# Kernel optimization log

Measured on AMD Instinct MI355X. Metric: run time of the kernel, lower is better.

## Reference

```python
import jax, jax.numpy as jnp
import numpy as np

N = 50000       # nodes
E_RAND = 800000 # random edges (avg degree ~16)
K = 64          # edges touching `node`; setup_inputs guarantees exactly K
F = 64          # num_node_features
C = 64          # conv_channels


def setup_inputs() -> dict:
    key = jax.random.key(0)
    ks = jax.random.split(key, 6)
    x = jax.random.normal(ks[0], (N, F), dtype=jnp.float32)
    # random edges avoiding node 0 so exactly the K prepended edges touch node 0
    src = jax.random.randint(ks[1], (E_RAND,), 1, N, dtype=jnp.int64)
    dst = jax.random.randint(ks[2], (E_RAND,), 1, N, dtype=jnp.int64)
    ksrc = jnp.zeros((K,), dtype=jnp.int64)
    kdst = jnp.arange(1, K + 1, dtype=jnp.int64)
    edge_index = jnp.stack([jnp.concatenate([ksrc, src]),
                            jnp.concatenate([kdst, dst])])  # [2, K+E_RAND]
    W1 = jax.random.normal(ks[3], (F, C), jnp.float32) / np.float32(np.sqrt(F))
    b1 = jnp.zeros((C,), jnp.float32)
    W2 = jax.random.normal(ks[4], (C, C), jnp.float32) / np.float32(np.sqrt(C))
    b2 = jnp.zeros((C,), jnp.float32)
    Wr = jax.random.normal(ks[5], (C, 1), jnp.float32) / np.float32(np.sqrt(C))
    br = jnp.zeros((1,), jnp.float32)
    return {"x": x, "edge_index": edge_index, "node": 0,
            "W1": W1, "b1": b1, "W2": W2, "b2": b2, "Wr": Wr, "br": br}


def gcn_conv(x, src, dst, W, b):
    """PyG GCNConv with self-loops already appended to (src, dst).
    out[v] = sum_{(u,v)} deg(u)^-1/2 * deg(v)^-1/2 * (x @ W)[u] + b
    """
    n = x.shape[0]
    xw = x @ W                                              # [N, C]
    deg = jnp.zeros((n,), xw.dtype).at[dst].add(1.0)        # in-degree incl. self-loop
    dinv = jnp.where(deg > 0, jax.lax.rsqrt(deg), 0.0)
    norm = dinv[src] * dinv[dst]                            # [E]
    out = jax.ops.segment_sum(xw[src] * norm[:, None], dst, num_segments=n)
    return out + b


def reference(x, edge_index, node, W1, b1, W2, b2, Wr, br):
    n = x.shape[0]
    loop = jnp.arange(n, dtype=edge_index.dtype)
    src = jnp.concatenate([edge_index[0], loop])  # add self loops (GCNConv default)
    dst = jnp.concatenate([edge_index[1], loop])
    h = jax.nn.relu(gcn_conv(x, src, dst, W1, b1))
    h = jax.nn.relu(gcn_conv(h, src, dst, W2, b2))
    # edges incident to `node` (setup guarantees exactly K such edges)
    s0, d0 = edge_index[0], edge_index[1]
    mask = (s0 == node) | (d0 == node)
    idx = jnp.nonzero(mask, size=K)[0]
    s, d = s0[idx], d0[idx]
    targets = jnp.where(s == node, d, s)  # self-loop (s==d==node) -> node
    score = h[targets] @ Wr + br          # [K, 1]
    score = jax.nn.softmax(score, axis=0)
    return score[:, 0], targets
```

## Files before the change

### kernel.cpp

```cpp
#include <hip/hip_runtime.h>
#include <math.h>

#define KK 64
#define CAP 64
#define NF 4160
#define HSZ 8192

__global__ __launch_bounds__(256) void k_find(const int* __restrict__ ei, int E,
                                              const int* __restrict__ nodep,
                                              int* __restrict__ cnt,
                                              int* __restrict__ tcount,
                                              int* __restrict__ tpairs,
                                              float* __restrict__ h1s) {
    int idx = blockIdx.x * 256 + threadIdx.x;
    if (idx < 64) h1s[(size_t)NF * 64 + idx] = 0.f;
    int node = nodep[0];
    int n4 = E >> 2;
    if (idx < n4) {
        int4 ss = ((const int4*)ei)[idx];
        int4 dd = ((const int4*)(ei + E))[idx];
        int s[4] = {ss.x, ss.y, ss.z, ss.w};
        int d[4] = {dd.x, dd.y, dd.z, dd.w};
#pragma unroll
        for (int k = 0; k < 4; k++) {
            atomicAdd(&cnt[d[k]], 1);
            if (s[k] == node || d[k] == node) {
                int q = atomicAdd(tcount, 1);
                if (q < KK) { int e = idx * 4 + k; tpairs[2 * q] = e; tpairs[2 * q + 1] = (s[k] == node) ? d[k] : s[k]; }
            }
        }
    }
    if (idx == 0) {
        for (int e = n4 * 4; e < E; e++) {
            int s = ei[e], d = ei[E + e];
            atomicAdd(&cnt[d], 1);
            if (s == node || d == node) {
                int q = atomicAdd(tcount, 1);
                if (q < KK) { tpairs[2 * q] = e; tpairs[2 * q + 1] = (s == node) ? d : s; }
            }
        }
    }
}

__global__ __launch_bounds__(256) void k_collect_t(const int* __restrict__ ei, int E,
                                                   const int* __restrict__ tpairs,
                                                   int* __restrict__ tcnt2,
                                                   int* __restrict__ tslots,
                                                   int* __restrict__ tsorted_g,
                                                   int* __restrict__ towner_g) {
    __shared__ unsigned char tflag[50048];
    __shared__ int eidx[KK], tgt[KK], srt[KK];
    int tid = threadIdx.x;
    for (int i = tid; i < 50048 / 16; i += 256) ((int4*)tflag)[i] = make_int4(0, 0, 0, 0);
    if (tid < KK) { eidx[tid] = tpairs[2 * tid]; tgt[tid] = tpairs[2 * tid + 1]; }
    __syncthreads();
    if (tid < KK) {
        int rank = 0;
        for (int j = 0; j < KK; j++) rank += (eidx[j] < eidx[tid]) ? 1 : 0;
        srt[rank] = tgt[tid];
    }
    __syncthreads();
    if (tid < KK) {
        int mynode = srt[tid];
        int owner = tid;
        for (int j = 0; j < tid; j++) if (srt[j] == mynode) { owner = j; break; }
        if (owner == tid) tflag[mynode] = (unsigned char)(tid + 1);
        if (blockIdx.x == 0) { tsorted_g[tid] = mynode; towner_g[tid] = owner; }
    }
    __syncthreads();
    int n4 = E >> 2;
    for (int idx = blockIdx.x * 256 + tid; idx < n4; idx += gridDim.x * 256) {
        int4 ss = ((const int4*)ei)[idx];
        int4 dd = ((const int4*)(ei + E))[idx];
        int s[4] = {ss.x, ss.y, ss.z, ss.w};
        int d[4] = {dd.x, dd.y, dd.z, dd.w};
#pragma unroll
        for (int k = 0; k < 4; k++) {
            int f = tflag[d[k]];
            if (f) { int p = atomicAdd(&tcnt2[f - 1], 1); if (p < CAP) tslots[(f - 1) * CAP + p] = s[k]; }
        }
    }
    if (blockIdx.x == 0 && tid == 0) {
        for (int e = n4 * 4; e < E; e++) {
            int f = tflag[ei[E + e]];
            if (f) { int p = atomicAdd(&tcnt2[f - 1], 1); if (p < CAP) tslots[(f - 1) * CAP + p] = ei[e]; }
        }
    }
}

__device__ __forceinline__ int fnode_of(int i, const int* tsorted, const int* towner,
                                        const int* tcnt2, const int* tslots) {
    int tp = i / 65, j = i % 65;
    if (j == 0) return tsorted[tp];
    int own = towner[tp];
    int c = tcnt2[own]; if (c > CAP) c = CAP;
    return (j - 1 < c) ? tslots[own * CAP + (j - 1)] : -1;
}

__global__ __launch_bounds__(256) void k_collect_f(const int* __restrict__ ei, int E,
                                                   const int* __restrict__ tsorted,
                                                   const int* __restrict__ towner,
                                                   const int* __restrict__ tcnt2,
                                                   const int* __restrict__ tslots,
                                                   int* __restrict__ fcnt,
                                                   int* __restrict__ fslots,
                                                   int* __restrict__ fnode_g,
                                                   int* __restrict__ fidx_g,
                                                   unsigned char* __restrict__ fown_g) {
    __shared__ unsigned int hmap[HSZ];
    int tid = threadIdx.x;
    for (int i = tid; i < HSZ; i += 256) hmap[i] = 0xFFFFFFFFu;
    __syncthreads();
    for (int i = tid; i < NF; i += 256) {
        int u = fnode_of(i, tsorted, towner, tcnt2, tslots);
        if (u >= 0) {
            unsigned int packed = ((unsigned)u << 16) | (unsigned)i;
            unsigned int slot = (((unsigned)u * 2654435761u) >> 13) & (HSZ - 1);
            while (true) {
                unsigned int cur = hmap[slot];
                if (cur == 0xFFFFFFFFu) {
                    unsigned int old = atomicCAS(&hmap[slot], 0xFFFFFFFFu, packed);
                    if (old == 0xFFFFFFFFu) break;
                    cur = old;
                }
                if ((cur >> 16) == (unsigned)u) {
                    if ((cur & 0xFFFFu) <= (unsigned)i) break;
                    if (atomicCAS(&hmap[slot], cur, packed) == cur) break;
                } else {
                    slot = (slot + 1) & (HSZ - 1);
                }
            }
        }
    }
    __syncthreads();
    if (blockIdx.x == 0) {
        for (int i = tid; i < NF; i += 256) {
            int u = fnode_of(i, tsorted, towner, tcnt2, tslots);
            int row = NF, isown = 0;
            if (u >= 0) {
                unsigned int slot = (((unsigned)u * 2654435761u) >> 13) & (HSZ - 1);
                while (true) {
                    unsigned int cur = hmap[slot];
                    if ((cur >> 16) == (unsigned)u) { row = (int)(cur & 0xFFFFu); break; }
                    slot = (slot + 1) & (HSZ - 1);
                }
                isown = (row == i);
            }
            fnode_g[i] = u; fidx_g[i] = row; fown_g[i] = (unsigned char)isown;
        }
    }
    int n4 = E >> 2;
    for (int idx = blockIdx.x * 256 + tid; idx < n4; idx += gridDim.x * 256) {
        int4 ss = ((const int4*)ei)[idx];
        int4 dd = ((const int4*)(ei + E))[idx];
        int s[4] = {ss.x, ss.y, ss.z, ss.w};
        int d[4] = {dd.x, dd.y, dd.z, dd.w};
#pragma unroll
        for (int k = 0; k < 4; k++) {
            unsigned int key = (unsigned)d[k];
            unsigned int slot = ((key * 2654435761u) >> 13) & (HSZ - 1);
            int row = -1;
            while (true) {
                unsigned int cur = hmap[slot];
                if (cur == 0xFFFFFFFFu) break;
                if ((cur >> 16) == key) { row = (int)(cur & 0xFFFFu); break; }
                slot = (slot + 1) & (HSZ - 1);
            }
            if (row >= 0) { int p = atomicAdd(&fcnt[row], 1); if (p < CAP) fslots[(size_t)row * CAP + p] = s[k]; }
        }
    }
    if (blockIdx.x == 0 && tid == 0) {
        for (int e = n4 * 4; e < E; e++) {
            unsigned int key = (unsigned)ei[E + e];
            unsigned int slot = ((key * 2654435761u) >> 13) & (HSZ - 1);
            int row = -1;
            while (true) {
                unsigned int cur = hmap[slot];
                if (cur == 0xFFFFFFFFu) break;
                if ((cur >> 16) == key) { row = (int)(cur & 0xFFFFu); break; }
                slot = (slot + 1) & (HSZ - 1);
            }
            if (row >= 0) { int p = atomicAdd(&fcnt[row], 1); if (p < CAP) fslots[(size_t)row * CAP + p] = ei[e]; }
        }
    }
}

__global__ __launch_bounds__(256) void k_layer1(const float* __restrict__ x,
                                                const int* __restrict__ fnode,
                                                const unsigned char* __restrict__ fown,
                                                const int* __restrict__ cnt,
                                                const int* __restrict__ fcnt,
                                                const int* __restrict__ fslots,
                                                const float* __restrict__ W1,
                                                const float* __restrict__ b1,
                                                float* __restrict__ h1s) {
    __shared__ __align__(16) float W1s[64 * 64];
    int tid = threadIdx.x;
    for (int i = tid; i < 1024; i += 256) ((float4*)W1s)[i] = ((const float4*)W1)[i];
    __syncthreads();
    int i = blockIdx.x * 4 + (tid >> 6);
    int lane = tid & 63;
    if (i >= NF) return;
    if (!fown[i]) return;
    int u = fnode[i];
    float du = rsqrtf((float)(cnt[u] + 1));
    float acc = du * x[(size_t)u * 64 + lane];
    int c = fcnt[i]; if (c > CAP) c = CAP;
    const int* sl = fslots + (size_t)i * CAP;
    int k = 0;
    for (; k + 4 <= c; k += 4) {
        int u0 = sl[k], u1 = sl[k + 1], u2 = sl[k + 2], u3 = sl[k + 3];
        float f0 = rsqrtf((float)(cnt[u0] + 1));
        float f1 = rsqrtf((float)(cnt[u1] + 1));
        float f2 = rsqrtf((float)(cnt[u2] + 1));
        float f3 = rsqrtf((float)(cnt[u3] + 1));
        acc += f0 * x[(size_t)u0 * 64 + lane] + f1 * x[(size_t)u1 * 64 + lane]
             + f2 * x[(size_t)u2 * 64 + lane] + f3 * x[(size_t)u3 * 64 + lane];
    }
    for (; k < c; k++) {
        int uu = sl[k];
        acc += rsqrtf((float)(cnt[uu] + 1)) * x[(size_t)uu * 64 + lane];
    }
    float z = du * acc;
    float h = 0.f;
#pragma unroll
    for (int f = 0; f < 64; f++) h += __shfl(z, f) * W1s[f * 64 + lane];
    h = fmaxf(h + b1[lane], 0.f);
    h1s[(size_t)i * 64 + lane] = du * h;
}

__global__ __launch_bounds__(64) void k_score2(const float* __restrict__ h1s,
                                               const int* __restrict__ fidx,
                                               const int* __restrict__ tsorted,
                                               const int* __restrict__ cnt,
                                               const float* __restrict__ W2,
                                               const float* __restrict__ b2,
                                               const float* __restrict__ Wr,
                                               float* __restrict__ sc) {
    int tp = blockIdx.x;
    int lane = threadIdx.x;
    int t = tsorted[tp];
    float dt = rsqrtf((float)(cnt[t] + 1));
    const int* fx = fidx + tp * 65;
    float z = 0.f;
#pragma unroll
    for (int j = 0; j < 65; j++) {
        int idx = fx[j];
        z += h1s[(size_t)idx * 64 + lane];
    }
    z *= dt;
    float acc = 0.f;
#pragma unroll
    for (int f = 0; f < 64; f++) acc += __shfl(z, f) * W2[f * 64 + lane];
    float h2 = fmaxf(acc + b2[lane], 0.f);
    float p = h2 * Wr[lane];
#pragma unroll
    for (int off = 32; off >= 1; off >>= 1) p += __shfl_xor(p, off);
    if (lane == 0) sc[tp] = p;
}

__global__ void k_softmax(const float* __restrict__ sc, const int* __restrict__ tsorted,
                          float* __restrict__ out) {
    int t = threadIdx.x;
    float s = sc[t];
    float m = s;
#pragma unroll
    for (int off = 32; off >= 1; off >>= 1) m = fmaxf(m, __shfl_xor(m, off));
    float e = __expf(s - m);
    float ss = e;
#pragma unroll
    for (int off = 32; off >= 1; off >>= 1) ss += __shfl_xor(ss, off);
    out[t] = e / ss;
    out[KK + t] = (float)tsorted[t];
}

extern "C" void kernel_launch(void* const* d_in, const int* in_sizes, int n_in,
                              void* d_out, int out_size, void* d_ws, size_t ws_size,
                              hipStream_t stream) {
    const float* x  = (const float*)d_in[0];
    const int*   ei = (const int*)d_in[1];
    const int*   nodep = (const int*)d_in[2];
    const float* W1 = (const float*)d_in[3];
    const float* b1 = (const float*)d_in[4];
    const float* W2 = (const float*)d_in[5];
    const float* b2 = (const float*)d_in[6];
    const float* Wr = (const float*)d_in[7];
    const float* br = (const float*)d_in[8];
    float* out = (float*)d_out;
    (void)br;

    int N = in_sizes[0] / 64;
    int E = in_sizes[1] / 2;

    char* w = (char*)d_ws;
    char* zstart = w;
    int* cnt    = (int*)w; w += (size_t)N * 4;
    int* tcnt2  = (int*)w; w += KK * 4;
    int* fcnt   = (int*)w; w += (size_t)NF * 4;
    int* tcount = (int*)w; w += 16;
    size_t zbytes = (size_t)(w - zstart);
    int* tpairs  = (int*)w; w += 2 * KK * 4;
    int* tsorted = (int*)w; w += KK * 4;
    int* towner  = (int*)w; w += KK * 4;
    int* tslots  = (int*)w; w += (size_t)KK * CAP * 4;
    int* fnode   = (int*)w; w += (size_t)NF * 4;
    int* fidx    = (int*)w; w += (size_t)NF * 4;
    unsigned char* fown = (unsigned char*)w; w += (size_t)NF;
    w = (char*)(((size_t)w + 15) & ~(size_t)15);
    int* fslots  = (int*)w; w += (size_t)NF * CAP * 4;
    float* h1s   = (float*)w; w += (size_t)(NF + 1) * 64 * 4;
    float* sc    = (float*)w; w += KK * 4;

    hipMemsetAsync(zstart, 0, zbytes, stream);

    int n4 = E >> 2;
    int ebl = (n4 + 255) / 256;
    k_find<<<ebl, 256, 0, stream>>>(ei, E, nodep, cnt, tcount, tpairs, h1s);
    k_collect_t<<<512, 256, 0, stream>>>(ei, E, tpairs, tcnt2, tslots, tsorted, towner);
    k_collect_f<<<512, 256, 0, stream>>>(ei, E, tsorted, towner, tcnt2, tslots,
                                         fcnt, fslots, fnode, fidx, fown);
    k_layer1<<<(NF + 3) / 4, 256, 0, stream>>>(x, fnode, fown, cnt, fcnt, fslots, W1, b1, h1s);
    k_score2<<<KK, 64, 0, stream>>>(h1s, fidx, tsorted, cnt, W2, b2, Wr, sc);
    k_softmax<<<1, 64, 0, stream>>>(sc, tsorted, out);
}
```

Before: 170.8 us.

## Fuse all stages into one cooperative persistent kernel with grid syncs

Replaces the memset plus six separate kernel launches with a single cooperative kernel of 256 blocks that runs every stage and separates them with grid.sync(). Workspace zeroing now happens inside the kernel. The goal is to remove launch gaps and the memset. In exchange, the edge-scan phases run on fewer blocks than before (256 instead of up to 512 or ~800), the large shared buffer limits occupancy, and the grid-wide barriers have their own cost.

```diff
diff --git a/kernel.cpp b/kernel.cpp
--- a/kernel.cpp
+++ b/kernel.cpp
@@ -1,92 +1,15 @@
 #include <hip/hip_runtime.h>
+#include <hip/hip_cooperative_groups.h>
 #include <math.h>
+
+namespace cg = cooperative_groups;
 
 #define KK 64
 #define CAP 64
 #define NF 4160
 #define HSZ 8192
-
-__global__ __launch_bounds__(256) void k_find(const int* __restrict__ ei, int E,
-                                              const int* __restrict__ nodep,
-                                              int* __restrict__ cnt,
-                                              int* __restrict__ tcount,
-                                              int* __restrict__ tpairs,
-                                              float* __restrict__ h1s) {
-    int idx = blockIdx.x * 256 + threadIdx.x;
-    if (idx < 64) h1s[(size_t)NF * 64 + idx] = 0.f;
-    int node = nodep[0];
-    int n4 = E >> 2;
-    if (idx < n4) {
-        int4 ss = ((const int4*)ei)[idx];
-        int4 dd = ((const int4*)(ei + E))[idx];
-        int s[4] = {ss.x, ss.y, ss.z, ss.w};
-        int d[4] = {dd.x, dd.y, dd.z, dd.w};
-#pragma unroll
-        for (int k = 0; k < 4; k++) {
-            atomicAdd(&cnt[d[k]], 1);
-            if (s[k] == node || d[k] == node) {
-                int q = atomicAdd(tcount, 1);
-                if (q < KK) { int e = idx * 4 + k; tpairs[2 * q] = e; tpairs[2 * q + 1] = (s[k] == node) ? d[k] : s[k]; }
-            }
-        }
-    }
-    if (idx == 0) {
-        for (int e = n4 * 4; e < E; e++) {
-            int s = ei[e], d = ei[E + e];
-            atomicAdd(&cnt[d], 1);
-            if (s == node || d == node) {
-                int q = atomicAdd(tcount, 1);
-                if (q < KK) { tpairs[2 * q] = e; tpairs[2 * q + 1] = (s == node) ? d : s; }
-            }
-        }
-    }
-}
-
-__global__ __launch_bounds__(256) void k_collect_t(const int* __restrict__ ei, int E,
-                                                   const int* __restrict__ tpairs,
-                                                   int* __restrict__ tcnt2,
-                                                   int* __restrict__ tslots,
-                                                   int* __restrict__ tsorted_g,
-                                                   int* __restrict__ towner_g) {
-    __shared__ unsigned char tflag[50048];
-    __shared__ int eidx[KK], tgt[KK], srt[KK];
-    int tid = threadIdx.x;
-    for (int i = tid; i < 50048 / 16; i += 256) ((int4*)tflag)[i] = make_int4(0, 0, 0, 0);
-    if (tid < KK) { eidx[tid] = tpairs[2 * tid]; tgt[tid] = tpairs[2 * tid + 1]; }
-    __syncthreads();
-    if (tid < KK) {
-        int rank = 0;
-        for (int j = 0; j < KK; j++) rank += (eidx[j] < eidx[tid]) ? 1 : 0;
-        srt[rank] = tgt[tid];
-    }
-    __syncthreads();
-    if (tid < KK) {
-        int mynode = srt[tid];
-        int owner = tid;
-        for (int j = 0; j < tid; j++) if (srt[j] == mynode) { owner = j; break; }
-        if (owner == tid) tflag[mynode] = (unsigned char)(tid + 1);
-        if (blockIdx.x == 0) { tsorted_g[tid] = mynode; towner_g[tid] = owner; }
-    }
-    __syncthreads();
-    int n4 = E >> 2;
-    for (int idx = blockIdx.x * 256 + tid; idx < n4; idx += gridDim.x * 256) {
-        int4 ss = ((const int4*)ei)[idx];
-        int4 dd = ((const int4*)(ei + E))[idx];
-        int s[4] = {ss.x, ss.y, ss.z, ss.w};
-        int d[4] = {dd.x, dd.y, dd.z, dd.w};
-#pragma unroll
-        for (int k = 0; k < 4; k++) {
-            int f = tflag[d[k]];
-            if (f) { int p = atomicAdd(&tcnt2[f - 1], 1); if (p < CAP) tslots[(f - 1) * CAP + p] = s[k]; }
-        }
-    }
-    if (blockIdx.x == 0 && tid == 0) {
-        for (int e = n4 * 4; e < E; e++) {
-            int f = tflag[ei[E + e]];
-            if (f) { int p = atomicAdd(&tcnt2[f - 1], 1); if (p < CAP) tslots[(f - 1) * CAP + p] = ei[e]; }
-        }
-    }
-}
+#define NB 256
+#define NT 256
 
 __device__ __forceinline__ int fnode_of(int i, const int* tsorted, const int* towner,
                                         const int* tcnt2, const int* tslots) {
@@ -97,181 +20,249 @@
     return (j - 1 < c) ? tslots[own * CAP + (j - 1)] : -1;
 }
 
-__global__ __launch_bounds__(256) void k_collect_f(const int* __restrict__ ei, int E,
-                                                   const int* __restrict__ tsorted,
-                                                   const int* __restrict__ towner,
-                                                   const int* __restrict__ tcnt2,
-                                                   const int* __restrict__ tslots,
-                                                   int* __restrict__ fcnt,
-                                                   int* __restrict__ fslots,
-                                                   int* __restrict__ fnode_g,
-                                                   int* __restrict__ fidx_g,
-                                                   unsigned char* __restrict__ fown_g) {
-    __shared__ unsigned int hmap[HSZ];
-    int tid = threadIdx.x;
-    for (int i = tid; i < HSZ; i += 256) hmap[i] = 0xFFFFFFFFu;
-    __syncthreads();
-    for (int i = tid; i < NF; i += 256) {
-        int u = fnode_of(i, tsorted, towner, tcnt2, tslots);
-        if (u >= 0) {
-            unsigned int packed = ((unsigned)u << 16) | (unsigned)i;
-            unsigned int slot = (((unsigned)u * 2654435761u) >> 13) & (HSZ - 1);
-            while (true) {
-                unsigned int cur = hmap[slot];
-                if (cur == 0xFFFFFFFFu) {
-                    unsigned int old = atomicCAS(&hmap[slot], 0xFFFFFFFFu, packed);
-                    if (old == 0xFFFFFFFFu) break;
-                    cur = old;
-                }
-                if ((cur >> 16) == (unsigned)u) {
-                    if ((cur & 0xFFFFu) <= (unsigned)i) break;
-                    if (atomicCAS(&hmap[slot], cur, packed) == cur) break;
-                } else {
-                    slot = (slot + 1) & (HSZ - 1);
-                }
-            }
-        }
-    }
-    __syncthreads();
-    if (blockIdx.x == 0) {
-        for (int i = tid; i < NF; i += 256) {
-            int u = fnode_of(i, tsorted, towner, tcnt2, tslots);
-            int row = NF, isown = 0;
-            if (u >= 0) {
-                unsigned int slot = (((unsigned)u * 2654435761u) >> 13) & (HSZ - 1);
-                while (true) {
-                    unsigned int cur = hmap[slot];
-                    if ((cur >> 16) == (unsigned)u) { row = (int)(cur & 0xFFFFu); break; }
-                    slot = (slot + 1) & (HSZ - 1);
-                }
-                isown = (row == i);
-            }
-            fnode_g[i] = u; fidx_g[i] = row; fown_g[i] = (unsigned char)isown;
-        }
-    }
+__global__ __launch_bounds__(NT) void k_mega(
+    const float* __restrict__ x, const int* __restrict__ ei, int E, int N,
+    const int* __restrict__ nodep,
+    const float* __restrict__ W1, const float* __restrict__ b1,
+    const float* __restrict__ W2, const float* __restrict__ b2,
+    const float* __restrict__ Wr,
+    int* cnt, int* tcount, int* tpairs,
+    int* tsorted_g, int* towner_g, int* tcnt2, int* tslots,
+    int* fnode_g, int* fidx_g, unsigned char* fown_g,
+    int* fcnt, int* fslots, float* h1s, float* sc, float* out)
+{
+    cg::grid_group grid = cg::this_grid();
+    __shared__ __align__(16) unsigned char smem[50048 + 1024];
+    int tid = threadIdx.x, bid = blockIdx.x;
+    int gidx = bid * NT + tid;
+    const int gstride = NB * NT;
     int n4 = E >> 2;
-    for (int idx = blockIdx.x * 256 + tid; idx < n4; idx += gridDim.x * 256) {
+
+    for (int i = gidx; i < N; i += gstride) cnt[i] = 0;
+    for (int i = gidx; i < NF; i += gstride) fcnt[i] = 0;
+    if (gidx < KK) tcnt2[gidx] = 0;
+    if (gidx == 0) *tcount = 0;
+    if (gidx < 64) h1s[(size_t)NF * 64 + gidx] = 0.f;
+    grid.sync();
+
+    int node = nodep[0];
+    for (int idx = gidx; idx < n4; idx += gstride) {
         int4 ss = ((const int4*)ei)[idx];
         int4 dd = ((const int4*)(ei + E))[idx];
         int s[4] = {ss.x, ss.y, ss.z, ss.w};
         int d[4] = {dd.x, dd.y, dd.z, dd.w};
 #pragma unroll
         for (int k = 0; k < 4; k++) {
-            unsigned int key = (unsigned)d[k];
-            unsigned int slot = ((key * 2654435761u) >> 13) & (HSZ - 1);
-            int row = -1;
-            while (true) {
-                unsigned int cur = hmap[slot];
-                if (cur == 0xFFFFFFFFu) break;
-                if ((cur >> 16) == key) { row = (int)(cur & 0xFFFFu); break; }
-                slot = (slot + 1) & (HSZ - 1);
-            }
-            if (row >= 0) { int p = atomicAdd(&fcnt[row], 1); if (p < CAP) fslots[(size_t)row * CAP + p] = s[k]; }
-        }
-    }
-    if (blockIdx.x == 0 && tid == 0) {
+            atomicAdd(&cnt[d[k]], 1);
+            if (s[k] == node || d[k] == node) {
+                int q = atomicAdd(tcount, 1);
+                if (q < KK) { int e = idx * 4 + k; tpairs[2 * q] = e; tpairs[2 * q + 1] = (s[k] == node) ? d[k] : s[k]; }
+            }
+        }
+    }
+    if (gidx == 0) {
         for (int e = n4 * 4; e < E; e++) {
-            unsigned int key = (unsigned)ei[E + e];
-            unsigned int slot = ((key * 2654435761u) >> 13) & (HSZ - 1);
-            int row = -1;
-            while (true) {
-                unsigned int cur = hmap[slot];
-                if (cur == 0xFFFFFFFFu) break;
-                if ((cur >> 16) == key) { row = (int)(cur & 0xFFFFu); break; }
-                slot = (slot + 1) & (HSZ - 1);
-            }
-            if (row >= 0) { int p = atomicAdd(&fcnt[row], 1); if (p < CAP) fslots[(size_t)row * CAP + p] = ei[e]; }
-        }
-    }
-}
-
-__global__ __launch_bounds__(256) void k_layer1(const float* __restrict__ x,
-                                                const int* __restrict__ fnode,
-                                                const unsigned char* __restrict__ fown,
-                                                const int* __restrict__ cnt,
-                                                const int* __restrict__ fcnt,
-                                                const int* __restrict__ fslots,
-                                                const float* __restrict__ W1,
-                                                const float* __restrict__ b1,
-                                                float* __restrict__ h1s) {
-    __shared__ __align__(16) float W1s[64 * 64];
-    int tid = threadIdx.x;
-    for (int i = tid; i < 1024; i += 256) ((float4*)W1s)[i] = ((const float4*)W1)[i];
-    __syncthreads();
-    int i = blockIdx.x * 4 + (tid >> 6);
-    int lane = tid & 63;
-    if (i >= NF) return;
-    if (!fown[i]) return;
-    int u = fnode[i];
-    float du = rsqrtf((float)(cnt[u] + 1));
-    float acc = du * x[(size_t)u * 64 + lane];
-    int c = fcnt[i]; if (c > CAP) c = CAP;
-    const int* sl = fslots + (size_t)i * CAP;
-    int k = 0;
-    for (; k + 4 <= c; k += 4) {
-        int u0 = sl[k], u1 = sl[k + 1], u2 = sl[k + 2], u3 = sl[k + 3];
-        float f0 = rsqrtf((float)(cnt[u0] + 1));
-        float f1 = rsqrtf((float)(cnt[u1] + 1));
-        float f2 = rsqrtf((float)(cnt[u2] + 1));
-        float f3 = rsqrtf((float)(cnt[u3] + 1));
-        acc += f0 * x[(size_t)u0 * 64 + lane] + f1 * x[(size_t)u1 * 64 + lane]
-             + f2 * x[(size_t)u2 * 64 + lane] + f3 * x[(size_t)u3 * 64 + lane];
-    }
-    for (; k < c; k++) {
-        int uu = sl[k];
-        acc += rsqrtf((float)(cnt[uu] + 1)) * x[(size_t)uu * 64 + lane];
-    }
-    float z = du * acc;
-    float h = 0.f;
-#pragma unroll
-    for (int f = 0; f < 64; f++) h += __shfl(z, f) * W1s[f * 64 + lane];
-    h = fmaxf(h + b1[lane], 0.f);
-    h1s[(size_t)i * 64 + lane] = du * h;
-}
-
-__global__ __launch_bounds__(64) void k_score2(const float* __restrict__ h1s,
-                                               const int* __restrict__ fidx,
-                                               const int* __restrict__ tsorted,
-                                               const int* __restrict__ cnt,
-                                               const float* __restrict__ W2,
-                                               const float* __restrict__ b2,
-                                               const float* __restrict__ Wr,
-                                               float* __restrict__ sc) {
-    int tp = blockIdx.x;
-    int lane = threadIdx.x;
-    int t = tsorted[tp];
-    float dt = rsqrtf((float)(cnt[t] + 1));
-    const int* fx = fidx + tp * 65;
-    float z = 0.f;
-#pragma unroll
-    for (int j = 0; j < 65; j++) {
-        int idx = fx[j];
-        z += h1s[(size_t)idx * 64 + lane];
-    }
-    z *= dt;
-    float acc = 0.f;
-#pragma unroll
-    for (int f = 0; f < 64; f++) acc += __shfl(z, f) * W2[f * 64 + lane];
-    float h2 = fmaxf(acc + b2[lane], 0.f);
-    float p = h2 * Wr[lane];
-#pragma unroll
-    for (int off = 32; off >= 1; off >>= 1) p += __shfl_xor(p, off);
-    if (lane == 0) sc[tp] = p;
-}
-
-__global__ void k_softmax(const float* __restrict__ sc, const int* __restrict__ tsorted,
-                          float* __restrict__ out) {
-    int t = threadIdx.x;
-    float s = sc[t];
-    float m = s;
-#pragma unroll
-    for (int off = 32; off >= 1; off >>= 1) m = fmaxf(m, __shfl_xor(m, off));
-    float e = __expf(s - m);
-    float ss = e;
-#pragma unroll
-    for (int off = 32; off >= 1; off >>= 1) ss += __shfl_xor(ss, off);
-    out[t] = e / ss;
-    out[KK + t] = (float)tsorted[t];
+            int s = ei[e], d = ei[E + e];
+            atomicAdd(&cnt[d], 1);
+            if (s == node || d == node) {
+                int q = atomicAdd(tcount, 1);
+                if (q < KK) { tpairs[2 * q] = e; tpairs[2 * q + 1] = (s == node) ? d : s; }
+            }
+        }
+    }
+    grid.sync();
+
+    {
+        unsigned char* tflag = smem;
+        int* eidx = (int*)(smem + 50048);
+        int* tgt = eidx + KK;
+        int* srt = tgt + KK;
+        for (int i = tid; i < 50048 / 16; i += NT) ((int4*)tflag)[i] = make_int4(0, 0, 0, 0);
+        if (tid < KK) { eidx[tid] = tpairs[2 * tid]; tgt[tid] = tpairs[2 * tid + 1]; }
+        __syncthreads();
+        if (tid < KK) {
+            int rank = 0;
+            for (int j = 0; j < KK; j++) rank += (eidx[j] < eidx[tid]) ? 1 : 0;
+            srt[rank] = tgt[tid];
+        }
+        __syncthreads();
+        if (tid < KK) {
+            int mynode = srt[tid];
+            int owner = tid;
+            for (int j = 0; j < tid; j++) if (srt[j] == mynode) { owner = j; break; }
+            if (owner == tid) tflag[mynode] = (unsigned char)(tid + 1);
+            if (bid == 0) { tsorted_g[tid] = mynode; towner_g[tid] = owner; }
+        }
+        __syncthreads();
+        for (int idx = gidx; idx < n4; idx += gstride) {
+            int4 ss = ((const int4*)ei)[idx];
+            int4 dd = ((const int4*)(ei + E))[idx];
+            int s[4] = {ss.x, ss.y, ss.z, ss.w};
+            int d[4] = {dd.x, dd.y, dd.z, dd.w};
+#pragma unroll
+            for (int k = 0; k < 4; k++) {
+                int f = tflag[d[k]];
+                if (f) { int p = atomicAdd(&tcnt2[f - 1], 1); if (p < CAP) tslots[(f - 1) * CAP + p] = s[k]; }
+            }
+        }
+        if (gidx == 0) {
+            for (int e = n4 * 4; e < E; e++) {
+                int f = tflag[ei[E + e]];
+                if (f) { int p = atomicAdd(&tcnt2[f - 1], 1); if (p < CAP) tslots[(f - 1) * CAP + p] = ei[e]; }
+            }
+        }
+    }
+    grid.sync();
+
+    {
+        unsigned int* hmap = (unsigned int*)smem;
+        for (int i = tid; i < HSZ; i += NT) hmap[i] = 0xFFFFFFFFu;
+        __syncthreads();
+        for (int i = tid; i < NF; i += NT) {
+            int u = fnode_of(i, tsorted_g, towner_g, tcnt2, tslots);
+            if (u >= 0) {
+                unsigned int packed = ((unsigned)u << 16) | (unsigned)i;
+                unsigned int slot = (((unsigned)u * 2654435761u) >> 13) & (HSZ - 1);
+                while (true) {
+                    unsigned int cur = hmap[slot];
+                    if (cur == 0xFFFFFFFFu) {
+                        unsigned int old = atomicCAS(&hmap[slot], 0xFFFFFFFFu, packed);
+                        if (old == 0xFFFFFFFFu) break;
+                        cur = old;
+                    }
+                    if ((cur >> 16) == (unsigned)u) {
+                        if ((cur & 0xFFFFu) <= (unsigned)i) break;
+                        if (atomicCAS(&hmap[slot], cur, packed) == cur) break;
+                    } else {
+                        slot = (slot + 1) & (HSZ - 1);
+                    }
+                }
+            }
+        }
+        __syncthreads();
+        if (bid == 0) {
+            for (int i = tid; i < NF; i += NT) {
+                int u = fnode_of(i, tsorted_g, towner_g, tcnt2, tslots);
+                int row = NF, isown = 0;
+                if (u >= 0) {
+                    unsigned int slot = (((unsigned)u * 2654435761u) >> 13) & (HSZ - 1);
+                    while (true) {
+                        unsigned int cur = hmap[slot];
+                        if ((cur >> 16) == (unsigned)u) { row = (int)(cur & 0xFFFFu); break; }
+                        slot = (slot + 1) & (HSZ - 1);
+                    }
+                    isown = (row == i);
+                }
+                fnode_g[i] = u; fidx_g[i] = row; fown_g[i] = (unsigned char)isown;
+            }
+        }
+        for (int idx = gidx; idx < n4; idx += gstride) {
+            int4 ss = ((const int4*)ei)[idx];
+            int4 dd = ((const int4*)(ei + E))[idx];
+            int s[4] = {ss.x, ss.y, ss.z, ss.w};
+            int d[4] = {dd.x, dd.y, dd.z, dd.w};
+#pragma unroll
+            for (int k = 0; k < 4; k++) {
+                unsigned int key = (unsigned)d[k];
+                unsigned int slot = ((key * 2654435761u) >> 13) & (HSZ - 1);
+                int row = -1;
+                while (true) {
+                    unsigned int cur = hmap[slot];
+                    if (cur == 0xFFFFFFFFu) break;
+                    if ((cur >> 16) == key) { row = (int)(cur & 0xFFFFu); break; }
+                    slot = (slot + 1) & (HSZ - 1);
+                }
+                if (row >= 0) { int p = atomicAdd(&fcnt[row], 1); if (p < CAP) fslots[(size_t)row * CAP + p] = s[k]; }
+            }
+        }
+        if (gidx == 0) {
+            for (int e = n4 * 4; e < E; e++) {
+                unsigned int key = (unsigned)ei[E + e];
+                unsigned int slot = ((key * 2654435761u) >> 13) & (HSZ - 1);
+                int row = -1;
+                while (true) {
+                    unsigned int cur = hmap[slot];
+                    if (cur == 0xFFFFFFFFu) break;
+                    if ((cur >> 16) == key) { row = (int)(cur & 0xFFFFu); break; }
+                    slot = (slot + 1) & (HSZ - 1);
+                }
+                if (row >= 0) { int p = atomicAdd(&fcnt[row], 1); if (p < CAP) fslots[(size_t)row * CAP + p] = ei[e]; }
+            }
+        }
+    }
+    grid.sync();
+
+    {
+        float* W1s = (float*)smem;
+        for (int i = tid; i < 1024; i += NT) ((float4*)W1s)[i] = ((const float4*)W1)[i];
+        __syncthreads();
+        int wv = tid >> 6, lane = tid & 63;
+        for (int i = bid * 4 + wv; i < NF; i += NB * 4) {
+            if (!fown_g[i]) continue;
+            int u = fnode_g[i];
+            float du = rsqrtf((float)(cnt[u] + 1));
+            float acc = du * x[(size_t)u * 64 + lane];
+            int c = fcnt[i]; if (c > CAP) c = CAP;
+            const int* sl = fslots + (size_t)i * CAP;
+            int k = 0;
+            for (; k + 4 <= c; k += 4) {
+                int u0 = sl[k], u1 = sl[k + 1], u2 = sl[k + 2], u3 = sl[k + 3];
+                float f0 = rsqrtf((float)(cnt[u0] + 1));
+                float f1 = rsqrtf((float)(cnt[u1] + 1));
+                float f2 = rsqrtf((float)(cnt[u2] + 1));
+                float f3 = rsqrtf((float)(cnt[u3] + 1));
+                acc += f0 * x[(size_t)u0 * 64 + lane] + f1 * x[(size_t)u1 * 64 + lane]
+                     + f2 * x[(size_t)u2 * 64 + lane] + f3 * x[(size_t)u3 * 64 + lane];
+            }
+            for (; k < c; k++) {
+                int uu = sl[k];
+                acc += rsqrtf((float)(cnt[uu] + 1)) * x[(size_t)uu * 64 + lane];
+            }
+            float z = du * acc;
+            float h = 0.f;
+#pragma unroll
+            for (int f = 0; f < 64; f++) h += __shfl(z, f) * W1s[f * 64 + lane];
+            h = fmaxf(h + b1[lane], 0.f);
+            h1s[(size_t)i * 64 + lane] = du * h;
+        }
+    }
+    grid.sync();
+
+    if (bid < KK && tid < 64) {
+        int tp = bid, lane = tid;
+        int t = tsorted_g[tp];
+        float dt = rsqrtf((float)(cnt[t] + 1));
+        const int* fx = fidx_g + tp * 65;
+        float z = 0.f;
+#pragma unroll
+        for (int j = 0; j < 65; j++) {
+            int idx = fx[j];
+            z += h1s[(size_t)idx * 64 + lane];
+        }
+        z *= dt;
+        float acc = 0.f;
+#pragma unroll
+        for (int f = 0; f < 64; f++) acc += __shfl(z, f) * W2[f * 64 + lane];
+        float h2 = fmaxf(acc + b2[lane], 0.f);
+        float p = h2 * Wr[lane];
+#pragma unroll
+        for (int off = 32; off >= 1; off >>= 1) p += __shfl_xor(p, off);
+        if (lane == 0) sc[tp] = p;
+    }
+    grid.sync();
+
+    if (bid == 0 && tid < KK) {
+        float s = sc[tid];
+        float m = s;
+#pragma unroll
+        for (int off = 32; off >= 1; off >>= 1) m = fmaxf(m, __shfl_xor(m, off));
+        float e = __expf(s - m);
+        float ss = e;
+#pragma unroll
+        for (int off = 32; off >= 1; off >>= 1) ss += __shfl_xor(ss, off);
+        out[tid] = e / ss;
+        out[KK + tid] = (float)tsorted_g[tid];
+    }
 }
 
 extern "C" void kernel_launch(void* const* d_in, const int* in_sizes, int n_in,
@@ -293,33 +284,27 @@
     int E = in_sizes[1] / 2;
 
     char* w = (char*)d_ws;
-    char* zstart = w;
-    int* cnt    = (int*)w; w += (size_t)N * 4;
-    int* tcnt2  = (int*)w; w += KK * 4;
-    int* fcnt   = (int*)w; w += (size_t)NF * 4;
-    int* tcount = (int*)w; w += 16;
-    size_t zbytes = (size_t)(w - zstart);
+    int* cnt     = (int*)w; w += (size_t)N * 4;
+    int* tcount  = (int*)w; w += 16;
     int* tpairs  = (int*)w; w += 2 * KK * 4;
     int* tsorted = (int*)w; w += KK * 4;
     int* towner  = (int*)w; w += KK * 4;
+    int* tcnt2   = (int*)w; w += KK * 4;
     int* tslots  = (int*)w; w += (size_t)KK * CAP * 4;
     int* fnode   = (int*)w; w += (size_t)NF * 4;
     int* fidx    = (int*)w; w += (size_t)NF * 4;
+    int* fcnt    = (int*)w; w += (size_t)NF * 4;
     unsigned char* fown = (unsigned char*)w; w += (size_t)NF;
     w = (char*)(((size_t)w + 15) & ~(size_t)15);
     int* fslots  = (int*)w; w += (size_t)NF * CAP * 4;
     float* h1s   = (float*)w; w += (size_t)(NF + 1) * 64 * 4;
     float* sc    = (float*)w; w += KK * 4;
 
-    hipMemsetAsync(zstart, 0, zbytes, stream);
-
-    int n4 = E >> 2;
-    int ebl = (n4 + 255) / 256;
-    k_find<<<ebl, 256, 0, stream>>>(ei, E, nodep, cnt, tcount, tpairs, h1s);
-    k_collect_t<<<512, 256, 0, stream>>>(ei, E, tpairs, tcnt2, tslots, tsorted, towner);
-    k_collect_f<<<512, 256, 0, stream>>>(ei, E, tsorted, towner, tcnt2, tslots,
-                                         fcnt, fslots, fnode, fidx, fown);
-    k_layer1<<<(NF + 3) / 4, 256, 0, stream>>>(x, fnode, fown, cnt, fcnt, fslots, W1, b1, h1s);
-    k_score2<<<KK, 64, 0, stream>>>(h1s, fidx, tsorted, cnt, W2, b2, Wr, sc);
-    k_softmax<<<1, 64, 0, stream>>>(sc, tsorted, out);
+    void* args[] = { (void*)&x, (void*)&ei, (void*)&E, (void*)&N, (void*)&nodep,
+                     (void*)&W1, (void*)&b1, (void*)&W2, (void*)&b2, (void*)&Wr,
+                     (void*)&cnt, (void*)&tcount, (void*)&tpairs,
+                     (void*)&tsorted, (void*)&towner, (void*)&tcnt2, (void*)&tslots,
+                     (void*)&fnode, (void*)&fidx, (void*)&fown,
+                     (void*)&fcnt, (void*)&fslots, (void*)&h1s, (void*)&sc, (void*)&out };
+    hipLaunchCooperativeKernel((const void*)k_mega, dim3(NB), dim3(NT), args, 0, stream);
 }
```

After: 332.8 us. +94.9%, slower.

## Split degree counting across collect kernels and shrink shared target flag to bitmask

Applied to the files above, without the earlier changes.

Moves the in-degree atomic counting out of the find kernel and splits it between the two collect kernels, each handling half of every int4 group, so the atomics overlap with edge scans that already happen. It replaces the 50KB byte flag array in shared memory with a 6KB bitmask plus a linear search over 64 target nodes, which should raise occupancy of the collect kernel. Zeroing of the count buffers is folded into the find kernel instead of a large memset. The risk is that the degree array is now read only after both collect kernels finish, and the bitmask hit path adds a 64-entry scan per hit.

```diff
diff --git a/kernel.cpp b/kernel.cpp
--- a/kernel.cpp
+++ b/kernel.cpp
@@ -5,14 +5,16 @@
 #define CAP 64
 #define NF 4160
 #define HSZ 8192
+#define BMW 1568
 
 __global__ __launch_bounds__(256) void k_find(const int* __restrict__ ei, int E,
                                               const int* __restrict__ nodep,
-                                              int* __restrict__ cnt,
+                                              int4* __restrict__ zbase, int zcount4,
                                               int* __restrict__ tcount,
                                               int* __restrict__ tpairs,
                                               float* __restrict__ h1s) {
     int idx = blockIdx.x * 256 + threadIdx.x;
+    if (idx < zcount4) zbase[idx] = make_int4(0, 0, 0, 0);
     if (idx < 64) h1s[(size_t)NF * 64 + idx] = 0.f;
     int node = nodep[0];
     int n4 = E >> 2;
@@ -23,7 +25,6 @@
         int d[4] = {dd.x, dd.y, dd.z, dd.w};
 #pragma unroll
         for (int k = 0; k < 4; k++) {
-            atomicAdd(&cnt[d[k]], 1);
             if (s[k] == node || d[k] == node) {
                 int q = atomicAdd(tcount, 1);
                 if (q < KK) { int e = idx * 4 + k; tpairs[2 * q] = e; tpairs[2 * q + 1] = (s[k] == node) ? d[k] : s[k]; }
@@ -33,7 +34,6 @@
     if (idx == 0) {
         for (int e = n4 * 4; e < E; e++) {
             int s = ei[e], d = ei[E + e];
-            atomicAdd(&cnt[d], 1);
             if (s == node || d == node) {
                 int q = atomicAdd(tcount, 1);
                 if (q < KK) { tpairs[2 * q] = e; tpairs[2 * q + 1] = (s == node) ? d : s; }
@@ -44,14 +44,16 @@
 
 __global__ __launch_bounds__(256) void k_collect_t(const int* __restrict__ ei, int E,
                                                    const int* __restrict__ tpairs,
+                                                   int* __restrict__ cnt,
                                                    int* __restrict__ tcnt2,
                                                    int* __restrict__ tslots,
                                                    int* __restrict__ tsorted_g,
                                                    int* __restrict__ towner_g) {
-    __shared__ unsigned char tflag[50048];
+    __shared__ unsigned int bmask[BMW];
+    __shared__ int tnode[KK];
     __shared__ int eidx[KK], tgt[KK], srt[KK];
     int tid = threadIdx.x;
-    for (int i = tid; i < 50048 / 16; i += 256) ((int4*)tflag)[i] = make_int4(0, 0, 0, 0);
+    for (int i = tid; i < BMW; i += 256) bmask[i] = 0u;
     if (tid < KK) { eidx[tid] = tpairs[2 * tid]; tgt[tid] = tpairs[2 * tid + 1]; }
     __syncthreads();
     if (tid < KK) {
@@ -64,7 +66,8 @@
         int mynode = srt[tid];
         int owner = tid;
         for (int j = 0; j < tid; j++) if (srt[j] == mynode) { owner = j; break; }
-        if (owner == tid) tflag[mynode] = (unsigned char)(tid + 1);
+        tnode[tid] = (owner == tid) ? mynode : -1;
+        if (owner == tid) atomicOr(&bmask[mynode >> 5], 1u << (mynode & 31));
         if (blockIdx.x == 0) { tsorted_g[tid] = mynode; towner_g[tid] = owner; }
     }
     __syncthreads();
@@ -74,16 +77,26 @@
         int4 dd = ((const int4*)(ei + E))[idx];
         int s[4] = {ss.x, ss.y, ss.z, ss.w};
         int d[4] = {dd.x, dd.y, dd.z, dd.w};
+        atomicAdd(&cnt[d[0]], 1);
+        atomicAdd(&cnt[d[1]], 1);
 #pragma unroll
         for (int k = 0; k < 4; k++) {
-            int f = tflag[d[k]];
-            if (f) { int p = atomicAdd(&tcnt2[f - 1], 1); if (p < CAP) tslots[(f - 1) * CAP + p] = s[k]; }
+            if ((bmask[d[k] >> 5] >> (d[k] & 31)) & 1u) {
+                int f = 0;
+                for (int j = 0; j < KK; j++) if (tnode[j] == d[k]) { f = j + 1; break; }
+                if (f) { int p = atomicAdd(&tcnt2[f - 1], 1); if (p < CAP) tslots[(f - 1) * CAP + p] = s[k]; }
+            }
         }
     }
     if (blockIdx.x == 0 && tid == 0) {
         for (int e = n4 * 4; e < E; e++) {
-            int f = tflag[ei[E + e]];
-            if (f) { int p = atomicAdd(&tcnt2[f - 1], 1); if (p < CAP) tslots[(f - 1) * CAP + p] = ei[e]; }
+            int d = ei[E + e];
+            atomicAdd(&cnt[d], 1);
+            if ((bmask[d >> 5] >> (d & 31)) & 1u) {
+                int f = 0;
+                for (int j = 0; j < KK; j++) if (tnode[j] == d) { f = j + 1; break; }
+                if (f) { int p = atomicAdd(&tcnt2[f - 1], 1); if (p < CAP) tslots[(f - 1) * CAP + p] = ei[e]; }
+            }
         }
     }
 }
@@ -102,6 +115,7 @@
                                                    const int* __restrict__ towner,
                                                    const int* __restrict__ tcnt2,
                                                    const int* __restrict__ tslots,
+                                                   int* __restrict__ cnt,
                                                    int* __restrict__ fcnt,
                                                    int* __restrict__ fslots,
                                                    int* __restrict__ fnode_g,
@@ -155,6 +169,8 @@
         int4 dd = ((const int4*)(ei + E))[idx];
         int s[4] = {ss.x, ss.y, ss.z, ss.w};
         int d[4] = {dd.x, dd.y, dd.z, dd.w};
+        atomicAdd(&cnt[d[2]], 1);
+        atomicAdd(&cnt[d[3]], 1);
 #pragma unroll
         for (int k = 0; k < 4; k++) {
             unsigned int key = (unsigned)d[k];
@@ -293,12 +309,11 @@
     int E = in_sizes[1] / 2;
 
     char* w = (char*)d_ws;
-    char* zstart = w;
     int* cnt    = (int*)w; w += (size_t)N * 4;
+    int* fcnt   = (int*)w; w += (size_t)NF * 4;
     int* tcnt2  = (int*)w; w += KK * 4;
-    int* fcnt   = (int*)w; w += (size_t)NF * 4;
+    int zcount4 = (N + NF + KK) / 4;
     int* tcount = (int*)w; w += 16;
-    size_t zbytes = (size_t)(w - zstart);
     int* tpairs  = (int*)w; w += 2 * KK * 4;
     int* tsorted = (int*)w; w += KK * 4;
     int* towner  = (int*)w; w += KK * 4;
@@ -311,14 +326,14 @@
     float* h1s   = (float*)w; w += (size_t)(NF + 1) * 64 * 4;
     float* sc    = (float*)w; w += KK * 4;
 
-    hipMemsetAsync(zstart, 0, zbytes, stream);
+    hipMemsetAsync(tcount, 0, 16, stream);
 
     int n4 = E >> 2;
     int ebl = (n4 + 255) / 256;
-    k_find<<<ebl, 256, 0, stream>>>(ei, E, nodep, cnt, tcount, tpairs, h1s);
-    k_collect_t<<<512, 256, 0, stream>>>(ei, E, tpairs, tcnt2, tslots, tsorted, towner);
+    k_find<<<ebl, 256, 0, stream>>>(ei, E, nodep, (int4*)cnt, zcount4, tcount, tpairs, h1s);
+    k_collect_t<<<512, 256, 0, stream>>>(ei, E, tpairs, cnt, tcnt2, tslots, tsorted, towner);
     k_collect_f<<<512, 256, 0, stream>>>(ei, E, tsorted, towner, tcnt2, tslots,
-                                         fcnt, fslots, fnode, fidx, fown);
+                                         cnt, fcnt, fslots, fnode, fidx, fown);
     k_layer1<<<(NF + 3) / 4, 256, 0, stream>>>(x, fnode, fown, cnt, fcnt, fslots, W1, b1, h1s);
     k_score2<<<KK, 64, 0, stream>>>(h1s, fidx, tsorted, cnt, W2, b2, Wr, sc);
     k_softmax<<<1, 64, 0, stream>>>(sc, tsorted, out);
```

Measured after the change: 166.6 us. 2.4% less time.
